# Performance work log

Measured on AMD Instinct MI355X. Metric: run time of the kernel, lower is better.

Reference implementation:

```python
import jax, jax.numpy as jnp
import numpy as np

HIDDEN = 768
NUM_HEADS = 8
NUM_CELLS = 16384
MAX_HDRS = 8
NUM_HEADERS = 512
LN_EPS = 1e-5


def setup_inputs() -> dict:
    key = jax.random.key(0)
    ks = jax.random.split(key, 16)
    s = 0.02
    D = HIDDEN
    return {
        "cell_value_embeddings": jax.random.normal(ks[0], (NUM_CELLS, D), jnp.float32),
        "header_embeddings": jax.random.normal(ks[1], (NUM_HEADERS, D), jnp.float32),
        "cell_to_header_map": jax.random.randint(ks[2], (NUM_CELLS, MAX_HDRS), 0, NUM_HEADERS),
        "cell_positions": jax.random.randint(ks[3], (NUM_CELLS, 2), 0, 100),
        # nn.MultiheadAttention params
        "in_proj_w": jax.random.normal(ks[4], (3 * D, D), jnp.float32) * s,
        "in_proj_b": jnp.zeros((3 * D,), jnp.float32),
        "out_w": jax.random.normal(ks[5], (D, D), jnp.float32) * s,
        "out_b": jnp.zeros((D,), jnp.float32),
        # positional embedding tables
        "row_emb": jax.random.normal(ks[6], (100, D), jnp.float32) * s,
        "col_emb": jax.random.normal(ks[7], (100, D), jnp.float32) * s,
        # fusion: Linear(2D->D) + LayerNorm
        "fus_w": jax.random.normal(ks[8], (D, 2 * D), jnp.float32) * s,
        "fus_b": jnp.zeros((D,), jnp.float32),
        "ln_g": jnp.ones((D,), jnp.float32),
        "ln_b": jnp.zeros((D,), jnp.float32),
    }


def _forward(cell_value_embeddings, header_embeddings, in_proj_w, in_proj_b,
             out_w, out_b, row_emb, col_emb, fus_w, fus_b, ln_g, ln_b,
             cell_to_header_map, cell_positions):
    N, D = cell_value_embeddings.shape
    H = cell_to_header_map.shape[1]
    nh, dh = NUM_HEADS, D // NUM_HEADS
    scale = 1.0 / (dh ** 0.5)

    pos = jnp.clip(cell_positions, 0, 99)
    cwp = cell_value_embeddings + row_emb[pos[:, 0]] + col_emb[pos[:, 1]]  # [N,D]

    ids = cell_to_header_map
    mask = ids >= 0                                   # [N,H] valid header slots
    hg = header_embeddings[jnp.where(mask, ids, 0)]   # [N,H,D] gathered K/V inputs

    Wq, Wk, Wv = jnp.split(in_proj_w, 3, axis=0)
    bq, bk, bv = jnp.split(in_proj_b, 3)
    q = (cwp @ Wq.T + bq).reshape(N, nh, dh)          # [N,a,d]
    k = (hg @ Wk.T + bk).reshape(N, H, nh, dh)        # [N,k,a,d]
    v = (hg @ Wv.T + bv).reshape(N, H, nh, dh)

    scores = jnp.einsum('nad,nkad->nak', q, k) * scale          # [N,a,k]
    scores = jnp.where(mask[:, None, :], scores, -1e9)
    attn = jax.nn.softmax(scores, axis=-1)
    attn = jnp.where(mask[:, None, :], attn, 0.0)
    ctx = jnp.einsum('nak,nkad->nad', attn, v).reshape(N, D)
    att_out = ctx @ out_w.T + out_b                    # [N,D]

    comb = jnp.concatenate([cwp, att_out], axis=-1)    # [N,2D]
    h = comb @ fus_w.T + fus_b
    mu = jnp.mean(h, axis=-1, keepdims=True)
    var = jnp.mean((h - mu) ** 2, axis=-1, keepdims=True)
    h = (h - mu) * jax.lax.rsqrt(var + LN_EPS) * ln_g + ln_b
    fused = jax.nn.relu(h)

    has = jnp.any(mask, axis=-1)                       # cells with >=1 valid header
    enriched = jnp.where(has[:, None], fused, cwp)
    weights = jnp.where(mask, attn.mean(axis=1), 0.0)  # head-averaged attn [N,H]
    return enriched, weights


def reference(cell_value_embeddings, header_embeddings, cell_to_header_map,
              cell_positions, in_proj_w, in_proj_b, out_w, out_b, row_emb,
              col_emb, fus_w, fus_b, ln_g, ln_b):
    return _forward(cell_value_embeddings, header_embeddings, in_proj_w,
                    in_proj_b, out_w, out_b, row_emb, col_emb, fus_w, fus_b,
                    ln_g, ln_b, cell_to_header_map, cell_positions)
```

## Files before the change

### kernel.cpp

```cpp
#include <hip/hip_runtime.h>
#include <hip/hip_bf16.h>

#define NCELLS 16384
#define DIM    768
#define NHEADS 8
#define DHEAD  96
#define MAXH   8
#define ND     (NCELLS * DIM)


using bf16 = __hip_bfloat16;
typedef short  short8  __attribute__((ext_vector_type(8)));
typedef short  short4v __attribute__((ext_vector_type(4)));
typedef float  floatx4 __attribute__((ext_vector_type(4)));

__device__ inline short f2b(float f) {
    bf16 h = __float2bfloat16(f);
    unsigned short u; __builtin_memcpy(&u, &h, 2); return (short)u;
}
__device__ inline float b2f(short u) {
    unsigned x = ((unsigned)(unsigned short)u) << 16;
    float f; __builtin_memcpy(&f, &x, 4); return f;
}

__device__ inline short8 ld8(const float* p) {
    floatx4 a = *reinterpret_cast<const floatx4*>(p);
    floatx4 b = *reinterpret_cast<const floatx4*>(p + 4);
    short8 o;
#pragma unroll
    for (int i = 0; i < 4; ++i) { o[i] = f2b(a[i]); o[i + 4] = f2b(b[i]); }
    return o;
}

__device__ __forceinline__ void cp16(const void* g, void* l) {
    __builtin_amdgcn_global_load_lds(
        (const __attribute__((address_space(1))) void*)g,
        (__attribute__((address_space(3))) void*)l, 16, 0, 0);
}

template <int DUAL, int COUT>
__global__ __launch_bounds__(256) void gemm_bf(
    const bf16* __restrict__ A, const bf16* __restrict__ A2,
    const bf16* __restrict__ W, int ldw,
    const float* __restrict__ bias,
    float* __restrict__ Cf, bf16* __restrict__ Cb, int K)
{
    __shared__ short As[128 * 64];
    __shared__ short Bs[128 * 64];
    const int tid = threadIdx.x, wave = tid >> 6, lane = tid & 63;
    const int id = blockIdx.x;
    const int m0 = (id & 127) * 128;
    const int n0 = (id >> 7) * 128;
    const int wr = (wave & 1) * 64, wc = (wave >> 1) * 64;
    const int fr = lane & 15, kg = lane >> 4;

    const int srow = lane >> 3;
    const int scol = (lane & 7) ^ srow;

    floatx4 acc[16];
#pragma unroll
    for (int i = 0; i < 16; ++i) acc[i] = (floatx4){0.f, 0.f, 0.f, 0.f};

    for (int k0 = 0; k0 < K; k0 += 64) {
        const bf16* Ak; int ka;
        if (!DUAL || k0 < DIM) { Ak = A;  ka = k0; }
        else                   { Ak = A2; ka = k0 - DIM; }

        __syncthreads();
#pragma unroll
        for (int i = 0; i < 4; ++i) {
            const int c = i * 4 + wave;
            const int row = c * 8 + srow;
            cp16(Ak + (size_t)(m0 + row) * DIM + ka + scol * 8,
                 &As[c * 512 + lane * 8]);
            cp16(W  + (size_t)(n0 + row) * ldw + k0 + scol * 8,
                 &Bs[c * 512 + lane * 8]);
        }
        __syncthreads();

#pragma unroll
        for (int kk = 0; kk < 2; ++kk) {
            short8 af[4], bfv[4];
#pragma unroll
            for (int i = 0; i < 4; ++i) {
                const int sa = ((kk * 4 + kg) ^ (fr & 7)) * 8;
                af[i]  = *reinterpret_cast<const short8*>(&As[(wr + i * 16 + fr) * 64 + sa]);
                bfv[i] = *reinterpret_cast<const short8*>(&Bs[(wc + i * 16 + fr) * 64 + sa]);
            }
#pragma unroll
            for (int i = 0; i < 4; ++i)
#pragma unroll
                for (int j = 0; j < 4; ++j)
                    acc[i * 4 + j] = __builtin_amdgcn_mfma_f32_16x16x32_bf16(
                        af[i], bfv[j], acc[i * 4 + j], 0, 0, 0);
        }
    }

    const int col_l = lane & 15, row_q = kg * 4;
#pragma unroll
    for (int j = 0; j < 4; ++j) {
        const int col = n0 + wc + j * 16 + col_l;
        const float bv = bias[col];
#pragma unroll
        for (int i = 0; i < 4; ++i) {
#pragma unroll
            for (int r = 0; r < 4; ++r) {
                const int row = m0 + wr + i * 16 + row_q + r;
                const float v = acc[i * 4 + j][r] + bv;
                if (COUT == 0) Cf[(size_t)row * DIM + col] = v;
                else           Cb[(size_t)row * DIM + col] = __float2bfloat16(v);
            }
        }
    }
}

__global__ __launch_bounds__(256) void prep_kernel(
    const float* __restrict__ ce, const int* __restrict__ pos,
    const float* __restrict__ re, const float* __restrict__ co,
    bf16* __restrict__ cwp_b,
    const float* __restrict__ in_proj_w, bf16* __restrict__ Wq_b,
    const float* __restrict__ fus_w,     bf16* __restrict__ Wf_b,
    const float* __restrict__ out_w, const float* __restrict__ out_b,
    const float* __restrict__ fus_b, float* __restrict__ bco,
    const float* __restrict__ hdr, const float* __restrict__ in_proj_b,
    bf16* __restrict__ HKV)
{
    __shared__ short As[64 * 40];
    __shared__ short Bs[64 * 40];
    const int b = blockIdx.x, tid = threadIdx.x;

    if (b < 6144) {
        const int gid  = b * 256 + tid;
        const int cell = gid / 96;
        const int off  = (gid % 96) * 8;
        int pr = pos[cell * 2 + 0]; pr = min(max(pr, 0), 99);
        int pc = pos[cell * 2 + 1]; pc = min(max(pc, 0), 99);
        const float* a = ce + (size_t)cell * DIM + off;
        const float* bb = re + (size_t)pr * DIM + off;
        const float* c = co + (size_t)pc * DIM + off;
        floatx4 a0 = *reinterpret_cast<const floatx4*>(a);
        floatx4 a1 = *reinterpret_cast<const floatx4*>(a + 4);
        floatx4 b0 = *reinterpret_cast<const floatx4*>(bb);
        floatx4 b1 = *reinterpret_cast<const floatx4*>(bb + 4);
        floatx4 c0 = *reinterpret_cast<const floatx4*>(c);
        floatx4 c1 = *reinterpret_cast<const floatx4*>(c + 4);
        short8 o;
#pragma unroll
        for (int i = 0; i < 4; ++i) {
            o[i]     = f2b(a0[i] + b0[i] + c0[i]);
            o[i + 4] = f2b(a1[i] + b1[i] + c1[i]);
        }
        *reinterpret_cast<short8*>((short*)cwp_b + (size_t)cell * DIM + off) = o;
    } else if (b < 6720) {
        const int i = (b - 6144) * 256 + tid;
        floatx4 v = *reinterpret_cast<const floatx4*>(in_proj_w + (size_t)i * 4);
        short4v o;
#pragma unroll
        for (int j = 0; j < 4; ++j) o[j] = f2b(v[j]);
        *reinterpret_cast<short4v*>((short*)Wq_b + (size_t)i * 4) = o;
    } else if (b < 7296) {
        const int i  = (b - 6720) * 256 + tid;
        const int e0 = i * 4;
        const int n  = e0 / 768;
        const int k  = e0 - n * 768;
        const size_t src = (size_t)n * 1536 + k;
        floatx4 v = *reinterpret_cast<const floatx4*>(fus_w + src);
        short4v o;
#pragma unroll
        for (int j = 0; j < 4; ++j) o[j] = f2b(v[j]);
        *reinterpret_cast<short4v*>((short*)Wf_b + src) = o;
    } else if (b < 7299) {
        const int n = (b - 7296) * 256 + tid;
        const float* wrow = fus_w + (size_t)n * 1536 + 768;
        float acc = fus_b[n];
#pragma unroll 4
        for (int m = 0; m < 768; m += 4) {
            floatx4 wv = *reinterpret_cast<const floatx4*>(wrow + m);
            floatx4 ob = *reinterpret_cast<const floatx4*>(out_b + m);
            acc += wv[0] * ob[0] + wv[1] * ob[1] + wv[2] * ob[2] + wv[3] * ob[3];
        }
        bco[n] = acc;
    } else if (b < 7491) {
        const int b2 = b - 7299;
        const int m0 = (b2 & 7) * 64, n0 = (b2 >> 3) * 64;
        const float* W = in_proj_w + (size_t)DIM * DIM;
        const float* bias = in_proj_b + DIM;
        const int wave = tid >> 6, lane = tid & 63;
        const int lr = tid >> 2, lc = (tid & 3) * 8;
        const int fr = lane & 15, fk = (lane >> 4) * 8;

        floatx4 acc[4];
#pragma unroll
        for (int i = 0; i < 4; ++i) acc[i] = (floatx4){0.f, 0.f, 0.f, 0.f};

        for (int k0 = 0; k0 < DIM; k0 += 32) {
            short8 av = ld8(hdr + (size_t)(m0 + lr) * DIM + k0 + lc);
            short8 wv = ld8(W   + (size_t)(n0 + lr) * DIM + k0 + lc);
            __syncthreads();
            *reinterpret_cast<short8*>(&As[lr * 40 + lc]) = av;
            *reinterpret_cast<short8*>(&Bs[lr * 40 + lc]) = wv;
            __syncthreads();
            short8 af = *reinterpret_cast<const short8*>(&As[(wave * 16 + fr) * 40 + fk]);
#pragma unroll
            for (int t = 0; t < 4; ++t) {
                short8 bfv = *reinterpret_cast<const short8*>(&Bs[(t * 16 + fr) * 40 + fk]);
                acc[t] = __builtin_amdgcn_mfma_f32_16x16x32_bf16(af, bfv, acc[t], 0, 0, 0);
            }
        }
        const int col_l = lane & 15, row_q = (lane >> 4) * 4;
#pragma unroll
        for (int t = 0; t < 4; ++t) {
            const int col = n0 + t * 16 + col_l;
            const float bv = bias[col];
#pragma unroll
            for (int r = 0; r < 4; ++r) {
                const int row = m0 + wave * 16 + row_q + r;
                HKV[(size_t)row * 1536 + col] = __float2bfloat16(acc[t][r] + bv);
            }
        }
    } else {
        const int b3 = b - 7491;
        const int n0  = (b3 % 12) * 64;
        const int k0t = (b3 / 12) * 64;
        const int wave = tid >> 6, lane = tid & 63;
        const int lr = tid >> 2, lc = (tid & 3) * 8;
        const int rr = tid >> 3, cb = (tid & 7) * 8;
        const int fr = lane & 15, fk = (lane >> 4) * 8;

        floatx4 acc[4];
#pragma unroll
        for (int i = 0; i < 4; ++i) acc[i] = (floatx4){0.f, 0.f, 0.f, 0.f};

        for (int r0 = 0; r0 < DIM; r0 += 32) {
            short8 av = ld8(fus_w + (size_t)(n0 + lr) * 1536 + 768 + r0 + lc);
            floatx4 w0 = *reinterpret_cast<const floatx4*>(
                out_w + (size_t)(r0 + rr) * DIM + k0t + cb);
            floatx4 w1 = *reinterpret_cast<const floatx4*>(
                out_w + (size_t)(r0 + rr) * DIM + k0t + cb + 4);
            __syncthreads();
            *reinterpret_cast<short8*>(&As[lr * 40 + lc]) = av;
#pragma unroll
            for (int e = 0; e < 4; ++e) {
                Bs[(cb + e) * 40 + rr]     = f2b(w0[e]);
                Bs[(cb + 4 + e) * 40 + rr] = f2b(w1[e]);
            }
            __syncthreads();
            short8 af = *reinterpret_cast<const short8*>(&As[(wave * 16 + fr) * 40 + fk]);
#pragma unroll
            for (int t = 0; t < 4; ++t) {
                short8 bfv = *reinterpret_cast<const short8*>(&Bs[(t * 16 + fr) * 40 + fk]);
                acc[t] = __builtin_amdgcn_mfma_f32_16x16x32_bf16(af, bfv, acc[t], 0, 0, 0);
            }
        }
        const int col_l = lane & 15, row_q = (lane >> 4) * 4;
#pragma unroll
        for (int t = 0; t < 4; ++t) {
            const int col = k0t + t * 16 + col_l;
#pragma unroll
            for (int r = 0; r < 4; ++r) {
                const int row = n0 + wave * 16 + row_q + r;
                Wf_b[(size_t)row * 1536 + 768 + col] = __float2bfloat16(acc[t][r]);
            }
        }
    }
}

__global__ __launch_bounds__(256) void attn_v_kernel(
    const bf16* __restrict__ q, bf16* __restrict__ ctx,
    const bf16* __restrict__ HKV, const int* __restrict__ map,
    float* __restrict__ wout)
{
    const int h = threadIdx.x >> 7;
    const int t = threadIdx.x & 127;
    const int cell = blockIdx.x * 2 + h;
    __shared__ float qs[2][DIM];
    __shared__ float sc[2][64];
    __shared__ float at[2][64];
    __shared__ int   ids[2][MAXH];
    __shared__ float msk[2][MAXH];

    if (t < MAXH) {
        int id = map[cell * MAXH + t];
        msk[h][t] = (id >= 0) ? 1.f : 0.f;
        ids[h][t] = (id >= 0) ? id : 0;
    }
    if (t < 96) {
        short8 qv = *reinterpret_cast<const short8*>((const short*)q + (size_t)cell * DIM + t * 8);
#pragma unroll
        for (int e = 0; e < 8; ++e) qs[h][t * 8 + e] = b2f(qv[e]);
    }
    __syncthreads();

    if (t < 64) {
        const int a = t >> 3, j = t & 7;
        const short* kp = (const short*)HKV + (size_t)ids[h][j] * 1536 + a * DHEAD;
        float s = 0.f;
#pragma unroll
        for (int c = 0; c < 12; ++c) {
            short8 kv = *reinterpret_cast<const short8*>(kp + c * 8);
#pragma unroll
            for (int e = 0; e < 8; ++e)
                s += qs[h][a * DHEAD + c * 8 + e] * b2f(kv[e]);
        }
        s *= 0.10206207261596577f;
        sc[h][t] = (msk[h][j] != 0.f) ? s : -1e9f;
    }
    __syncthreads();

    if (t < NHEADS) {
        float m = -3e38f;
        for (int j = 0; j < MAXH; ++j) m = fmaxf(m, sc[h][t * 8 + j]);
        float e[MAXH]; float sum = 0.f;
        for (int j = 0; j < MAXH; ++j) { e[j] = expf(sc[h][t * 8 + j] - m); sum += e[j]; }
        const float inv = 1.f / sum;
        for (int j = 0; j < MAXH; ++j)
            at[h][t * 8 + j] = (msk[h][j] != 0.f) ? e[j] * inv : 0.f;
    }
    __syncthreads();

    if (t < MAXH) {
        float s = 0.f;
        for (int a = 0; a < NHEADS; ++a) s += at[h][a * 8 + t];
        wout[(size_t)cell * MAXH + t] = s * 0.125f;
    }

    if (t < 96) {
        const int a = t / 12, d0 = t * 8;
        float acc[8];
#pragma unroll
        for (int e = 0; e < 8; ++e) acc[e] = 0.f;
#pragma unroll
        for (int j = 0; j < MAXH; ++j) {
            short8 vv = *reinterpret_cast<const short8*>(
                (const short*)HKV + (size_t)ids[h][j] * 1536 + DIM + d0);
            const float w = at[h][a * 8 + j];
#pragma unroll
            for (int e = 0; e < 8; ++e) acc[e] += w * b2f(vv[e]);
        }
        short8 o;
#pragma unroll
        for (int e = 0; e < 8; ++e) o[e] = f2b(acc[e]);
        *reinterpret_cast<short8*>((short*)ctx + (size_t)cell * DIM + d0) = o;
    }
}

__global__ __launch_bounds__(384) void ln_v_kernel(
    float* io, const int* __restrict__ map,
    const float* __restrict__ ce, const int* __restrict__ pos,
    const float* __restrict__ re, const float* __restrict__ co,
    const float* __restrict__ g, const float* __restrict__ b)
{
    const int h = threadIdx.x / 192;
    const int t = threadIdx.x % 192;
    const int cell = blockIdx.x * 2 + h;
    const int wave = t >> 6, lane = t & 63;
    __shared__ float ws_[2][3], wq_[2][3];
    __shared__ int hasf[2];
    if (threadIdx.x < 2) hasf[threadIdx.x] = 0;

    float* hp = io + (size_t)cell * DIM;
    floatx4 v = *reinterpret_cast<const floatx4*>(hp + t * 4);
    float s  = v[0] + v[1] + v[2] + v[3];
    float q2 = v[0]*v[0] + v[1]*v[1] + v[2]*v[2] + v[3]*v[3];
#pragma unroll
    for (int off = 32; off > 0; off >>= 1) {
        s  += __shfl_down(s, off);
        q2 += __shfl_down(q2, off);
    }
    __syncthreads();
    if (t < MAXH && map[cell * MAXH + t] >= 0) hasf[h] = 1;
    if (lane == 0) { ws_[h][wave] = s; wq_[h][wave] = q2; }
    __syncthreads();

    const float mu  = (ws_[h][0] + ws_[h][1] + ws_[h][2]) * (1.f / 768.f);
    const float var = (wq_[h][0] + wq_[h][1] + wq_[h][2]) * (1.f / 768.f) - mu * mu;
    const float inv = rsqrtf(var + 1e-5f);

    if (hasf[h]) {
        floatx4 gv = *reinterpret_cast<const floatx4*>(g + t * 4);
        floatx4 bv = *reinterpret_cast<const floatx4*>(b + t * 4);
        floatx4 o;
#pragma unroll
        for (int e = 0; e < 4; ++e)
            o[e] = fmaxf((v[e] - mu) * inv * gv[e] + bv[e], 0.f);
        *reinterpret_cast<floatx4*>(hp + t * 4) = o;
    } else {
        int pr = pos[cell * 2 + 0]; pr = min(max(pr, 0), 99);
        int pc = pos[cell * 2 + 1]; pc = min(max(pc, 0), 99);
        floatx4 a0 = *reinterpret_cast<const floatx4*>(ce + (size_t)cell * DIM + t * 4);
        floatx4 b0 = *reinterpret_cast<const floatx4*>(re + (size_t)pr * DIM + t * 4);
        floatx4 c0 = *reinterpret_cast<const floatx4*>(co + (size_t)pc * DIM + t * 4);
        floatx4 o;
#pragma unroll
        for (int e = 0; e < 4; ++e) o[e] = a0[e] + b0[e] + c0[e];
        *reinterpret_cast<floatx4*>(hp + t * 4) = o;
    }
}

extern "C" void kernel_launch(void* const* d_in, const int* in_sizes, int n_in,
                              void* d_out, int out_size, void* d_ws, size_t ws_size,
                              hipStream_t stream) {
    (void)in_sizes; (void)n_in; (void)out_size; (void)ws_size;

    const float* cell_emb  = (const float*)d_in[0];
    const float* hdr_emb   = (const float*)d_in[1];
    const int*   map       = (const int*)d_in[2];
    const int*   pos       = (const int*)d_in[3];
    const float* in_proj_w = (const float*)d_in[4];
    const float* in_proj_b = (const float*)d_in[5];
    const float* out_w     = (const float*)d_in[6];
    const float* out_b     = (const float*)d_in[7];
    const float* row_emb   = (const float*)d_in[8];
    const float* col_emb   = (const float*)d_in[9];
    const float* fus_w     = (const float*)d_in[10];
    const float* fus_b     = (const float*)d_in[11];
    const float* ln_g      = (const float*)d_in[12];
    const float* ln_b      = (const float*)d_in[13];
    float* out = (float*)d_out;

    char* ws = (char*)d_ws;
    bf16*  HKV   = (bf16*)ws;
    bf16*  ctx_b = (bf16*)(ws + 1572864);
    bf16*  cwp_b = (bf16*)(ws + 26738688);
    bf16*  Wq_b  = (bf16*)(ws + 51904512);
    float* bco   = (float*)(ws + 53084160);
    bf16*  Wf_b  = (bf16*)(ws + 54263808);
    bf16* q_b = (bf16*)d_out;

    prep_kernel<<<7635, 256, 0, stream>>>(
        cell_emb, pos, row_emb, col_emb, cwp_b,
        in_proj_w, Wq_b, fus_w, Wf_b,
        out_w, out_b, fus_b, bco,
        hdr_emb, in_proj_b, HKV);

    gemm_bf<0, 1><<<768, 256, 0, stream>>>(
        cwp_b, nullptr, Wq_b, DIM, in_proj_b, nullptr, q_b, DIM);

    attn_v_kernel<<<NCELLS / 2, 256, 0, stream>>>(q_b, ctx_b, HKV, map, out + ND);

    gemm_bf<1, 0><<<768, 256, 0, stream>>>(
        cwp_b, ctx_b, Wf_b, 1536, bco, out, nullptr, 1536);

    ln_v_kernel<<<NCELLS / 2, 384, 0, stream>>>(out, map, cell_emb, pos,
                                                row_emb, col_emb, ln_g, ln_b);
}
```

Before: 293.2 us.

## Rewrite attention as one-wave-per-cell with shuffles; reorder prep blocks, widen K tiles

The attention kernel now gives each wavefront one cell and does scores, softmax, head-averaged weights and the context reduction with lane shuffles. This removes shared memory, block barriers and the idle threads of the old two-cells-per-block layout. In the prep kernel, the two small weight GEMM branches are moved to the lowest block indices so they start first instead of trailing the large elementwise work. Those GEMMs also use 64-wide K tiles with register prefetch of the next tile. The cost is more shuffle traffic and larger LDS tiles per block.

```diff
diff --git a/kernel.cpp b/kernel.cpp
--- a/kernel.cpp
+++ b/kernel.cpp
@@ -125,12 +125,156 @@
     const float* __restrict__ hdr, const float* __restrict__ in_proj_b,
     bf16* __restrict__ HKV)
 {
-    __shared__ short As[64 * 40];
-    __shared__ short Bs[64 * 40];
+    __shared__ short As[64 * 72];
+    __shared__ short Bs[64 * 72];
     const int b = blockIdx.x, tid = threadIdx.x;
 
-    if (b < 6144) {
-        const int gid  = b * 256 + tid;
+    if (b < 192) {
+        const int m0 = (b & 7) * 64, n0 = (b >> 3) * 64;
+        const float* W = in_proj_w + (size_t)DIM * DIM;
+        const float* bias = in_proj_b + DIM;
+        const int wave = tid >> 6, lane = tid & 63;
+        const int lr = tid >> 2, lc = (tid & 3) * 16;
+        const int fr = lane & 15, fk = (lane >> 4) * 8;
+
+        floatx4 acc[4];
+#pragma unroll
+        for (int i = 0; i < 4; ++i) acc[i] = (floatx4){0.f, 0.f, 0.f, 0.f};
+
+        const float* ap = hdr + (size_t)(m0 + lr) * DIM + lc;
+        const float* wp = W   + (size_t)(n0 + lr) * DIM + lc;
+        short8 a0 = ld8(ap), a1 = ld8(ap + 8);
+        short8 w0 = ld8(wp), w1 = ld8(wp + 8);
+
+        for (int it = 0; it < 12; ++it) {
+            __syncthreads();
+            *reinterpret_cast<short8*>(&As[lr * 72 + lc])     = a0;
+            *reinterpret_cast<short8*>(&As[lr * 72 + lc + 8]) = a1;
+            *reinterpret_cast<short8*>(&Bs[lr * 72 + lc])     = w0;
+            *reinterpret_cast<short8*>(&Bs[lr * 72 + lc + 8]) = w1;
+            __syncthreads();
+            if (it < 11) {
+                const int k0 = (it + 1) * 64;
+                a0 = ld8(ap + k0); a1 = ld8(ap + k0 + 8);
+                w0 = ld8(wp + k0); w1 = ld8(wp + k0 + 8);
+            }
+#pragma unroll
+            for (int kk = 0; kk < 2; ++kk) {
+                short8 af = *reinterpret_cast<const short8*>(
+                    &As[(wave * 16 + fr) * 72 + kk * 32 + fk]);
+#pragma unroll
+                for (int t = 0; t < 4; ++t) {
+                    short8 bfv = *reinterpret_cast<const short8*>(
+                        &Bs[(t * 16 + fr) * 72 + kk * 32 + fk]);
+                    acc[t] = __builtin_amdgcn_mfma_f32_16x16x32_bf16(af, bfv, acc[t], 0, 0, 0);
+                }
+            }
+        }
+        const int col_l = lane & 15, row_q = (lane >> 4) * 4;
+#pragma unroll
+        for (int t = 0; t < 4; ++t) {
+            const int col = n0 + t * 16 + col_l;
+            const float bv = bias[col];
+#pragma unroll
+            for (int r = 0; r < 4; ++r) {
+                const int row = m0 + wave * 16 + row_q + r;
+                HKV[(size_t)row * 1536 + col] = __float2bfloat16(acc[t][r] + bv);
+            }
+        }
+    } else if (b < 336) {
+        const int b3 = b - 192;
+        const int n0  = (b3 % 12) * 64;
+        const int k0t = (b3 / 12) * 64;
+        const int wave = tid >> 6, lane = tid & 63;
+        const int lr = tid >> 2, lc = (tid & 3) * 16;
+        const int fr = lane & 15, fk = (lane >> 4) * 8;
+
+        floatx4 acc[4];
+#pragma unroll
+        for (int i = 0; i < 4; ++i) acc[i] = (floatx4){0.f, 0.f, 0.f, 0.f};
+
+        const float* ap = fus_w + (size_t)(n0 + lr) * 1536 + 768 + lc;
+        const float* bp = out_w + (size_t)lr * DIM + k0t + lc;
+        short8 a0 = ld8(ap), a1 = ld8(ap + 8);
+        floatx4 q0 = *reinterpret_cast<const floatx4*>(bp);
+        floatx4 q1 = *reinterpret_cast<const floatx4*>(bp + 4);
+        floatx4 q2 = *reinterpret_cast<const floatx4*>(bp + 8);
+        floatx4 q3 = *reinterpret_cast<const floatx4*>(bp + 12);
+
+        for (int it = 0; it < 12; ++it) {
+            __syncthreads();
+            *reinterpret_cast<short8*>(&As[lr * 72 + lc])     = a0;
+            *reinterpret_cast<short8*>(&As[lr * 72 + lc + 8]) = a1;
+#pragma unroll
+            for (int e = 0; e < 4; ++e) {
+                Bs[(lc + e) * 72 + lr]      = f2b(q0[e]);
+                Bs[(lc + 4 + e) * 72 + lr]  = f2b(q1[e]);
+                Bs[(lc + 8 + e) * 72 + lr]  = f2b(q2[e]);
+                Bs[(lc + 12 + e) * 72 + lr] = f2b(q3[e]);
+            }
+            __syncthreads();
+            if (it < 11) {
+                const int r0 = (it + 1) * 64;
+                a0 = ld8(ap + r0); a1 = ld8(ap + r0 + 8);
+                const float* bq = bp + (size_t)r0 * DIM;
+                q0 = *reinterpret_cast<const floatx4*>(bq);
+                q1 = *reinterpret_cast<const floatx4*>(bq + 4);
+                q2 = *reinterpret_cast<const floatx4*>(bq + 8);
+                q3 = *reinterpret_cast<const floatx4*>(bq + 12);
+            }
+#pragma unroll
+            for (int kk = 0; kk < 2; ++kk) {
+                short8 af = *reinterpret_cast<const short8*>(
+                    &As[(wave * 16 + fr) * 72 + kk * 32 + fk]);
+#pragma unroll
+                for (int t = 0; t < 4; ++t) {
+                    short8 bfv = *reinterpret_cast<const short8*>(
+                        &Bs[(t * 16 + fr) * 72 + kk * 32 + fk]);
+                    acc[t] = __builtin_amdgcn_mfma_f32_16x16x32_bf16(af, bfv, acc[t], 0, 0, 0);
+                }
+            }
+        }
+        const int col_l = lane & 15, row_q = (lane >> 4) * 4;
+#pragma unroll
+        for (int t = 0; t < 4; ++t) {
+            const int col = k0t + t * 16 + col_l;
+#pragma unroll
+            for (int r = 0; r < 4; ++r) {
+                const int row = n0 + wave * 16 + row_q + r;
+                Wf_b[(size_t)row * 1536 + 768 + col] = __float2bfloat16(acc[t][r]);
+            }
+        }
+    } else if (b < 339) {
+        const int n = (b - 336) * 256 + tid;
+        const float* wrow = fus_w + (size_t)n * 1536 + 768;
+        float acc = fus_b[n];
+#pragma unroll 4
+        for (int m = 0; m < 768; m += 4) {
+            floatx4 wv = *reinterpret_cast<const floatx4*>(wrow + m);
+            floatx4 ob = *reinterpret_cast<const floatx4*>(out_b + m);
+            acc += wv[0] * ob[0] + wv[1] * ob[1] + wv[2] * ob[2] + wv[3] * ob[3];
+        }
+        bco[n] = acc;
+    } else if (b < 915) {
+        const int i = (b - 339) * 256 + tid;
+        floatx4 v = *reinterpret_cast<const floatx4*>(in_proj_w + (size_t)i * 4);
+        short4v o;
+#pragma unroll
+        for (int j = 0; j < 4; ++j) o[j] = f2b(v[j]);
+        *reinterpret_cast<short4v*>((short*)Wq_b + (size_t)i * 4) = o;
+    } else if (b < 1491) {
+        const int i  = (b - 915) * 256 + tid;
+        const int e0 = i * 4;
+        const int n  = e0 / 768;
+        const int k  = e0 - n * 768;
+        const size_t src = (size_t)n * 1536 + k;
+        floatx4 v = *reinterpret_cast<const floatx4*>(fus_w + src);
+        short4v o;
+#pragma unroll
+        for (int j = 0; j < 4; ++j) o[j] = f2b(v[j]);
+        *reinterpret_cast<short4v*>((short*)Wf_b + src) = o;
+    } else {
+        const int gid  = (b - 1491) * 256 + tid;
         const int cell = gid / 96;
         const int off  = (gid % 96) * 8;
         int pr = pos[cell * 2 + 0]; pr = min(max(pr, 0), 99);
@@ -151,196 +295,96 @@
             o[i + 4] = f2b(a1[i] + b1[i] + c1[i]);
         }
         *reinterpret_cast<short8*>((short*)cwp_b + (size_t)cell * DIM + off) = o;
-    } else if (b < 6720) {
-        const int i = (b - 6144) * 256 + tid;
-        floatx4 v = *reinterpret_cast<const floatx4*>(in_proj_w + (size_t)i * 4);
-        short4v o;
-#pragma unroll
-        for (int j = 0; j < 4; ++j) o[j] = f2b(v[j]);
-        *reinterpret_cast<short4v*>((short*)Wq_b + (size_t)i * 4) = o;
-    } else if (b < 7296) {
-        const int i  = (b - 6720) * 256 + tid;
-        const int e0 = i * 4;
-        const int n  = e0 / 768;
-        const int k  = e0 - n * 768;
-        const size_t src = (size_t)n * 1536 + k;
-        floatx4 v = *reinterpret_cast<const floatx4*>(fus_w + src);
-        short4v o;
-#pragma unroll
-        for (int j = 0; j < 4; ++j) o[j] = f2b(v[j]);
-        *reinterpret_cast<short4v*>((short*)Wf_b + src) = o;
-    } else if (b < 7299) {
-        const int n = (b - 7296) * 256 + tid;
-        const float* wrow = fus_w + (size_t)n * 1536 + 768;
-        float acc = fus_b[n];
-#pragma unroll 4
-        for (int m = 0; m < 768; m += 4) {
-            floatx4 wv = *reinterpret_cast<const floatx4*>(wrow + m);
-            floatx4 ob = *reinterpret_cast<const floatx4*>(out_b + m);
-            acc += wv[0] * ob[0] + wv[1] * ob[1] + wv[2] * ob[2] + wv[3] * ob[3];
-        }
-        bco[n] = acc;
-    } else if (b < 7491) {
-        const int b2 = b - 7299;
-        const int m0 = (b2 & 7) * 64, n0 = (b2 >> 3) * 64;
-        const float* W = in_proj_w + (size_t)DIM * DIM;
-        const float* bias = in_proj_b + DIM;
-        const int wave = tid >> 6, lane = tid & 63;
-        const int lr = tid >> 2, lc = (tid & 3) * 8;
-        const int fr = lane & 15, fk = (lane >> 4) * 8;
-
-        floatx4 acc[4];
-#pragma unroll
-        for (int i = 0; i < 4; ++i) acc[i] = (floatx4){0.f, 0.f, 0.f, 0.f};
-
-        for (int k0 = 0; k0 < DIM; k0 += 32) {
-            short8 av = ld8(hdr + (size_t)(m0 + lr) * DIM + k0 + lc);
-            short8 wv = ld8(W   + (size_t)(n0 + lr) * DIM + k0 + lc);
-            __syncthreads();
-            *reinterpret_cast<short8*>(&As[lr * 40 + lc]) = av;
-            *reinterpret_cast<short8*>(&Bs[lr * 40 + lc]) = wv;
-            __syncthreads();
-            short8 af = *reinterpret_cast<const short8*>(&As[(wave * 16 + fr) * 40 + fk]);
-#pragma unroll
-            for (int t = 0; t < 4; ++t) {
-                short8 bfv = *reinterpret_cast<const short8*>(&Bs[(t * 16 + fr) * 40 + fk]);
-                acc[t] = __builtin_amdgcn_mfma_f32_16x16x32_bf16(af, bfv, acc[t], 0, 0, 0);
-            }
-        }
-        const int col_l = lane & 15, row_q = (lane >> 4) * 4;
-#pragma unroll
-        for (int t = 0; t < 4; ++t) {
-            const int col = n0 + t * 16 + col_l;
-            const float bv = bias[col];
-#pragma unroll
-            for (int r = 0; r < 4; ++r) {
-                const int row = m0 + wave * 16 + row_q + r;
-                HKV[(size_t)row * 1536 + col] = __float2bfloat16(acc[t][r] + bv);
-            }
-        }
-    } else {
-        const int b3 = b - 7491;
-        const int n0  = (b3 % 12) * 64;
-        const int k0t = (b3 / 12) * 64;
-        const int wave = tid >> 6, lane = tid & 63;
-        const int lr = tid >> 2, lc = (tid & 3) * 8;
-        const int rr = tid >> 3, cb = (tid & 7) * 8;
-        const int fr = lane & 15, fk = (lane >> 4) * 8;
-
-        floatx4 acc[4];
-#pragma unroll
-        for (int i = 0; i < 4; ++i) acc[i] = (floatx4){0.f, 0.f, 0.f, 0.f};
-
-        for (int r0 = 0; r0 < DIM; r0 += 32) {
-            short8 av = ld8(fus_w + (size_t)(n0 + lr) * 1536 + 768 + r0 + lc);
-            floatx4 w0 = *reinterpret_cast<const floatx4*>(
-                out_w + (size_t)(r0 + rr) * DIM + k0t + cb);
-            floatx4 w1 = *reinterpret_cast<const floatx4*>(
-                out_w + (size_t)(r0 + rr) * DIM + k0t + cb + 4);
-            __syncthreads();
-            *reinterpret_cast<short8*>(&As[lr * 40 + lc]) = av;
-#pragma unroll
-            for (int e = 0; e < 4; ++e) {
-                Bs[(cb + e) * 40 + rr]     = f2b(w0[e]);
-                Bs[(cb + 4 + e) * 40 + rr] = f2b(w1[e]);
-            }
-            __syncthreads();
-            short8 af = *reinterpret_cast<const short8*>(&As[(wave * 16 + fr) * 40 + fk]);
-#pragma unroll
-            for (int t = 0; t < 4; ++t) {
-                short8 bfv = *reinterpret_cast<const short8*>(&Bs[(t * 16 + fr) * 40 + fk]);
-                acc[t] = __builtin_amdgcn_mfma_f32_16x16x32_bf16(af, bfv, acc[t], 0, 0, 0);
-            }
-        }
-        const int col_l = lane & 15, row_q = (lane >> 4) * 4;
-#pragma unroll
-        for (int t = 0; t < 4; ++t) {
-            const int col = k0t + t * 16 + col_l;
-#pragma unroll
-            for (int r = 0; r < 4; ++r) {
-                const int row = n0 + wave * 16 + row_q + r;
-                Wf_b[(size_t)row * 1536 + 768 + col] = __float2bfloat16(acc[t][r]);
-            }
-        }
-    }
-}
-
-__global__ __launch_bounds__(256) void attn_v_kernel(
+    }
+}
+
+__global__ __launch_bounds__(256) void attn_w_kernel(
     const bf16* __restrict__ q, bf16* __restrict__ ctx,
     const bf16* __restrict__ HKV, const int* __restrict__ map,
     float* __restrict__ wout)
 {
-    const int h = threadIdx.x >> 7;
-    const int t = threadIdx.x & 127;
-    const int cell = blockIdx.x * 2 + h;
-    __shared__ float qs[2][DIM];
-    __shared__ float sc[2][64];
-    __shared__ float at[2][64];
-    __shared__ int   ids[2][MAXH];
-    __shared__ float msk[2][MAXH];
-
-    if (t < MAXH) {
-        int id = map[cell * MAXH + t];
-        msk[h][t] = (id >= 0) ? 1.f : 0.f;
-        ids[h][t] = (id >= 0) ? id : 0;
-    }
-    if (t < 96) {
-        short8 qv = *reinterpret_cast<const short8*>((const short*)q + (size_t)cell * DIM + t * 8);
-#pragma unroll
-        for (int e = 0; e < 8; ++e) qs[h][t * 8 + e] = b2f(qv[e]);
-    }
-    __syncthreads();
-
-    if (t < 64) {
-        const int a = t >> 3, j = t & 7;
-        const short* kp = (const short*)HKV + (size_t)ids[h][j] * 1536 + a * DHEAD;
-        float s = 0.f;
-#pragma unroll
-        for (int c = 0; c < 12; ++c) {
-            short8 kv = *reinterpret_cast<const short8*>(kp + c * 8);
-#pragma unroll
-            for (int e = 0; e < 8; ++e)
-                s += qs[h][a * DHEAD + c * 8 + e] * b2f(kv[e]);
-        }
-        s *= 0.10206207261596577f;
-        sc[h][t] = (msk[h][j] != 0.f) ? s : -1e9f;
-    }
-    __syncthreads();
-
-    if (t < NHEADS) {
-        float m = -3e38f;
-        for (int j = 0; j < MAXH; ++j) m = fmaxf(m, sc[h][t * 8 + j]);
-        float e[MAXH]; float sum = 0.f;
-        for (int j = 0; j < MAXH; ++j) { e[j] = expf(sc[h][t * 8 + j] - m); sum += e[j]; }
-        const float inv = 1.f / sum;
-        for (int j = 0; j < MAXH; ++j)
-            at[h][t * 8 + j] = (msk[h][j] != 0.f) ? e[j] * inv : 0.f;
-    }
-    __syncthreads();
-
-    if (t < MAXH) {
-        float s = 0.f;
-        for (int a = 0; a < NHEADS; ++a) s += at[h][a * 8 + t];
-        wout[(size_t)cell * MAXH + t] = s * 0.125f;
-    }
-
-    if (t < 96) {
-        const int a = t / 12, d0 = t * 8;
+    const int wave = threadIdx.x >> 6, lane = threadIdx.x & 63;
+    const int cell = blockIdx.x * 4 + wave;
+    const int a = lane >> 3, j = lane & 7;
+
+    int id = map[(size_t)cell * MAXH + j];
+    const float msk = (id >= 0) ? 1.f : 0.f;
+    id = (id >= 0) ? id : 0;
+
+    const short* kp = (const short*)HKV + (size_t)id * 1536 + a * DHEAD;
+    const short* qp = (const short*)q + (size_t)cell * DIM + a * DHEAD;
+    float s = 0.f;
+#pragma unroll
+    for (int c = 0; c < 12; ++c) {
+        short8 kv = *reinterpret_cast<const short8*>(kp + c * 8);
+        short8 qv = *reinterpret_cast<const short8*>(qp + c * 8);
+#pragma unroll
+        for (int e = 0; e < 8; ++e) s += b2f(qv[e]) * b2f(kv[e]);
+    }
+    s *= 0.10206207261596577f;
+    s = (msk != 0.f) ? s : -1e9f;
+
+    float m = s;
+    m = fmaxf(m, __shfl_xor(m, 1));
+    m = fmaxf(m, __shfl_xor(m, 2));
+    m = fmaxf(m, __shfl_xor(m, 4));
+    float e = expf(s - m) * msk;
+    float sum = e;
+    sum += __shfl_xor(sum, 1);
+    sum += __shfl_xor(sum, 2);
+    sum += __shfl_xor(sum, 4);
+    const float at = (sum > 0.f) ? e / sum : 0.f;
+
+    float wsum = at;
+    wsum += __shfl_xor(wsum, 8);
+    wsum += __shfl_xor(wsum, 16);
+    wsum += __shfl_xor(wsum, 32);
+    if (lane < 8) wout[(size_t)cell * MAXH + lane] = wsum * 0.125f;
+
+    int vid[8];
+#pragma unroll
+    for (int jj = 0; jj < 8; ++jj) vid[jj] = __shfl(id, jj);
+
+    {
+        const int d0 = lane * 8;
+        const int ha = lane / 12;
         float acc[8];
 #pragma unroll
-        for (int e = 0; e < 8; ++e) acc[e] = 0.f;
-#pragma unroll
-        for (int j = 0; j < MAXH; ++j) {
+        for (int e2 = 0; e2 < 8; ++e2) acc[e2] = 0.f;
+#pragma unroll
+        for (int jj = 0; jj < 8; ++jj) {
+            const float w = __shfl(at, ha * 8 + jj);
             short8 vv = *reinterpret_cast<const short8*>(
-                (const short*)HKV + (size_t)ids[h][j] * 1536 + DIM + d0);
-            const float w = at[h][a * 8 + j];
-#pragma unroll
-            for (int e = 0; e < 8; ++e) acc[e] += w * b2f(vv[e]);
+                (const short*)HKV + (size_t)vid[jj] * 1536 + DIM + d0);
+#pragma unroll
+            for (int e2 = 0; e2 < 8; ++e2) acc[e2] += w * b2f(vv[e2]);
         }
         short8 o;
 #pragma unroll
-        for (int e = 0; e < 8; ++e) o[e] = f2b(acc[e]);
+        for (int e2 = 0; e2 < 8; ++e2) o[e2] = f2b(acc[e2]);
         *reinterpret_cast<short8*>((short*)ctx + (size_t)cell * DIM + d0) = o;
+    }
+
+    {
+        const int d0 = 512 + (lane & 31) * 8;
+        const int ha = d0 / 96;
+        float acc[8];
+#pragma unroll
+        for (int e2 = 0; e2 < 8; ++e2) acc[e2] = 0.f;
+#pragma unroll
+        for (int jj = 0; jj < 8; ++jj) {
+            const float w = __shfl(at, ha * 8 + jj);
+            short8 vv = *reinterpret_cast<const short8*>(
+                (const short*)HKV + (size_t)vid[jj] * 1536 + DIM + d0);
+#pragma unroll
+            for (int e2 = 0; e2 < 8; ++e2) acc[e2] += w * b2f(vv[e2]);
+        }
+        if (lane < 32) {
+            short8 o;
+#pragma unroll
+            for (int e2 = 0; e2 < 8; ++e2) o[e2] = f2b(acc[e2]);
+            *reinterpret_cast<short8*>((short*)ctx + (size_t)cell * DIM + d0) = o;
+        }
     }
 }
 
@@ -436,7 +480,7 @@
     gemm_bf<0, 1><<<768, 256, 0, stream>>>(
         cwp_b, nullptr, Wq_b, DIM, in_proj_b, nullptr, q_b, DIM);
 
-    attn_v_kernel<<<NCELLS / 2, 256, 0, stream>>>(q_b, ctx_b, HKV, map, out + ND);
+    attn_w_kernel<<<NCELLS / 4, 256, 0, stream>>>(q_b, ctx_b, HKV, map, out + ND);
 
     gemm_bf<1, 0><<<768, 256, 0, stream>>>(
         cwp_b, ctx_b, Wf_b, 1536, bco, out, nullptr, 1536);
```

New measurement: 314.9 us. +7.4%, slower.
